# Optimization experiments

Measured on AMD Instinct MI355X. Metric: run time of the kernel, lower is better.

The kernel has to match this reference:

```python
import jax, jax.numpy as jnp
import numpy as np

N_SITES = 100000
DIM = 128
KSIZE = 7  # 7^3 = 343 offsets
GRID = 160


def _build_sparse_structure(seed=0):
    """Sample N_SITES unique voxels in a GRID^3 volume and build the
    depthwise-conv kernel map: neighbor_idx[i, k] = index of site at
    coords[i] + offset[k], or N_SITES (sentinel -> zero row) if absent."""
    rng = np.random.default_rng(seed)
    lin = rng.choice(GRID ** 3, size=N_SITES, replace=False)
    coords = np.stack(np.unravel_index(lin, (GRID, GRID, GRID)), axis=1).astype(np.int64)  # [N,3]
    lookup = np.full(GRID ** 3, N_SITES, dtype=np.int32)
    lookup[lin] = np.arange(N_SITES, dtype=np.int32)
    r = KSIZE // 2
    offs = np.stack(np.meshgrid(*([np.arange(-r, r + 1)] * 3), indexing="ij"), axis=-1).reshape(-1, 3)  # [343,3]
    K = offs.shape[0]
    neighbor_idx = np.full((N_SITES, K), N_SITES, dtype=np.int32)
    for k in range(K):
        nb = coords + offs[k]
        ok = np.all((nb >= 0) & (nb < GRID), axis=1)
        nb_lin = (nb[ok, 0] * GRID + nb[ok, 1]) * GRID + nb[ok, 2]
        neighbor_idx[ok, k] = lookup[nb_lin]
    return neighbor_idx


def setup_inputs() -> dict:
    key = jax.random.key(0)
    ks = jax.random.split(key, 12)
    neighbor_idx = jnp.asarray(_build_sparse_structure(0))
    d, h = DIM, 4 * DIM
    K = KSIZE ** 3
    return {
        "feats": jax.random.normal(ks[0], (N_SITES, d), jnp.float32),
        "neighbor_idx": neighbor_idx,
        "dw_w": jax.random.normal(ks[1], (K, d), jnp.float32) * 0.05,
        "dw_b": jax.random.normal(ks[2], (d,), jnp.float32) * 0.02,
        "ln_g": 1.0 + 0.1 * jax.random.normal(ks[3], (d,), jnp.float32),
        "ln_b": 0.02 * jax.random.normal(ks[4], (d,), jnp.float32),
        "w1": jax.random.normal(ks[5], (d, h), jnp.float32) * (1.0 / np.sqrt(d)),
        "b1": 0.02 * jax.random.normal(ks[6], (h,), jnp.float32),
        "grn_g": 0.1 * jax.random.normal(ks[7], (1, h), jnp.float32),
        "grn_b": 0.02 * jax.random.normal(ks[8], (1, h), jnp.float32),
        "w2": jax.random.normal(ks[9], (h, d), jnp.float32) * (1.0 / np.sqrt(h)),
        "b2": 0.02 * jax.random.normal(ks[10], (d,), jnp.float32),
    }


def reference(feats, neighbor_idx, dw_w, dw_b, ln_g, ln_b, w1, b1, grn_g, grn_b, w2, b2):
    eps = 1e-6
    n, d = feats.shape
    # --- sparse depthwise conv: gather-multiply-accumulate over kernel offsets ---
    f_pad = jnp.concatenate([feats, jnp.zeros((1, d), feats.dtype)], axis=0)  # sentinel row

    def step(acc, xs):
        idx_k, w_k = xs  # idx_k: [N], w_k: [dim]
        return acc + f_pad[idx_k] * w_k, None

    x, _ = jax.lax.scan(step, jnp.zeros_like(feats), (neighbor_idx.T, dw_w))
    x = x + dw_b
    # --- LayerNorm over channels ---
    mu = jnp.mean(x, axis=-1, keepdims=True)
    var = jnp.var(x, axis=-1, keepdims=True)
    x = (x - mu) / jnp.sqrt(var + eps) * ln_g + ln_b
    # --- pwconv1 -> GELU (exact, matching torch default) ---
    x = jax.nn.gelu(x @ w1 + b1, approximate=False)  # [N, 4*dim]
    # --- GRN: L2 norm over all sites (dim=0), per channel ---
    gx = jnp.sqrt(jnp.sum(x * x, axis=0, keepdims=True))  # [1, 4*dim]
    nx = gx / (jnp.mean(gx, axis=-1, keepdims=True) + eps)
    x = grn_g * (x * nx) + grn_b + x
    # --- pwconv2 + residual (drop_path identity in eval) ---
    x = x @ w2 + b2
    return feats + x
```

## Files before the change

kernel.cpp:

```cpp
#include <hip/hip_runtime.h>

typedef unsigned short u16;
typedef unsigned int u32;
typedef __attribute__((ext_vector_type(8))) short bf16x8;
typedef __attribute__((ext_vector_type(4))) float f32x4;

__device__ __forceinline__ u16 f2bf(float f) {
    u32 u = __float_as_uint(f);
    return (u16)((u + 0x7FFFu + ((u >> 16) & 1u)) >> 16);
}

__device__ __forceinline__ float fast_gelu(float x) {
    const float t = x * x;
    const float y2 = x * __builtin_fmaf(0.0713548214f, t, 1.5957691216057308f);
    const float u = __expf(fminf(y2, 80.f));
    return x * u * __builtin_amdgcn_rcpf(u + 1.f);
}

__device__ __forceinline__ void gload_lds16(const u16* g, u16* l) {
    __builtin_amdgcn_global_load_lds(
        (const __attribute__((address_space(1))) void*)g,
        (__attribute__((address_space(3))) void*)l, 16, 0, 0);
}

__global__ __launch_bounds__(256) void cast_feats_k(
    const float* __restrict__ src, u16* __restrict__ dst, int n4)
{
    const int e = blockIdx.x * 256 + threadIdx.x;
    if (e >= n4) return;
    const float4 v = *(const float4*)(src + (size_t)e * 4);
    uint2 o;
    o.x = (u32)f2bf(v.x) | ((u32)f2bf(v.y) << 16);
    o.y = (u32)f2bf(v.z) | ((u32)f2bf(v.w) << 16);
    *(uint2*)(dst + (size_t)e * 4) = o;
}

__global__ __launch_bounds__(256) void dwln_k(
    const u16* __restrict__ featsb, const int* __restrict__ nb,
    const u16* __restrict__ dwwb, const float* __restrict__ dw_b,
    const float* __restrict__ ln_g, const float* __restrict__ ln_b,
    u16* __restrict__ xln, int nsites)
{
    __shared__ int lists[4][352];
    const int w = threadIdx.x >> 6;
    const int lane = threadIdx.x & 63;
    const int s = blockIdx.x * 4 + w;
    if (s >= nsites) return;
    const int* row = nb + (size_t)s * 343;
    int idx[6];
    #pragma unroll
    for (int j = 0; j < 5; ++j) idx[j] = row[lane + j * 64];
    idx[5] = (lane < 23) ? row[320 + lane] : nsites;
    const unsigned long long below = ((1ull << lane) - 1ull);
    int cnt = 0;
    #pragma unroll
    for (int i = 0; i < 6; ++i) {
        const bool v = idx[i] < nsites;
        const unsigned long long bal = __ballot(v);
        const int k = (i < 5) ? (lane + i * 64) : (320 + lane);
        if (v) lists[w][cnt + __popcll(bal & below)] = idx[i] | (k << 17);
        cnt += (int)__popcll(bal);
    }
    const int cntp = (cnt + 7) & ~7;
    if (lane < cntp - cnt) lists[w][cnt + lane] = nsites;
    __builtin_amdgcn_s_waitcnt(0);
    float x0 = 0.f, x1 = 0.f;
    for (int base = 0; base < cntp; base += 8) {
        u32 f[8], wv[8];
        #pragma unroll
        for (int i = 0; i < 8; ++i) {
            const int e = lists[w][base + i];
            f[i]  = *(const u32*)(featsb + (size_t)(e & 0x1FFFF) * 128 + lane * 2);
            wv[i] = *(const u32*)(dwwb + (size_t)(e >> 17) * 128 + lane * 2);
        }
        #pragma unroll
        for (int i = 0; i < 8; ++i) {
            x0 += __uint_as_float(f[i] << 16) * __uint_as_float(wv[i] << 16);
            x1 += __uint_as_float(f[i] & 0xFFFF0000u) * __uint_as_float(wv[i] & 0xFFFF0000u);
        }
    }
    const float2 bv = *(const float2*)(dw_b + lane * 2);
    const float2 gv = *(const float2*)(ln_g + lane * 2);
    const float2 lbv = *(const float2*)(ln_b + lane * 2);
    float a0 = x0 + bv.x, a1 = x1 + bv.y;
    float sm = a0 + a1, ss = a0 * a0 + a1 * a1;
    #pragma unroll
    for (int off = 32; off > 0; off >>= 1) {
        sm += __shfl_xor(sm, off, 64);
        ss += __shfl_xor(ss, off, 64);
    }
    const float mean = sm * (1.f / 128.f);
    const float var = ss * (1.f / 128.f) - mean * mean;
    const float rstd = rsqrtf(fmaxf(var, 0.f) + 1e-6f);
    const float y0 = (a0 - mean) * rstd * gv.x + lbv.x;
    const float y1 = (a1 - mean) * rstd * gv.y + lbv.y;
    *(u32*)(xln + (size_t)s * 128 + lane * 2) =
        (u32)f2bf(y0) | ((u32)f2bf(y1) << 16);
}

__global__ __launch_bounds__(256) void transpose_w1_k(
    const float* __restrict__ w1, u16* __restrict__ w1t)
{
    const int e = blockIdx.x * 256 + threadIdx.x;
    const int n = e >> 7, k = e & 127;
    w1t[e] = f2bf(w1[k * 512 + n]);
}

__global__ __launch_bounds__(256, 4) void gemm1_k(
    const u16* __restrict__ xln, const u16* __restrict__ w1t,
    const float* __restrict__ b1, u16* __restrict__ h,
    float* __restrict__ gx_sq, int nsites, int nmb)
{
    __shared__ u16 xb[2][64 * 128];
    __shared__ float s_red[128];
    const int t = threadIdx.x;
    const int n0 = blockIdx.x * 128;
    const int lane = t & 63;
    const int w = t >> 6;
    const int wn = w * 32;
    const int l15 = lane & 15, quad = lane >> 4;
    if (t < 128) s_red[t] = 0.f;

    #define STAGE1(bsel, mb_)                                                    \
        {                                                                        \
            _Pragma("unroll")                                                    \
            for (int i_ = 0; i_ < 4; ++i_) {                                     \
                const int r_ = w * 16 + i_ * 4 + (lane >> 4);                    \
                const int c_ = (lane & 15) ^ (r_ & 15);                          \
                gload_lds16(xln + (size_t)((mb_) * 64 + r_) * 128 + c_ * 8,      \
                            &xb[bsel][(w * 16 + i_ * 4) * 128]);                 \
            }                                                                    \
        }

    int mb = blockIdx.y;
    STAGE1(0, mb)
    __builtin_amdgcn_sched_barrier(0);
    const u16* a_base = w1t + (size_t)(n0 + wn + l15) * 128 + quad * 8;
    bf16x8 aF[4][2];
    #pragma unroll
    for (int ks = 0; ks < 4; ++ks)
        #pragma unroll
        for (int nt = 0; nt < 2; ++nt)
            aF[ks][nt] = *(const bf16x8*)(a_base + (size_t)nt * 16 * 128 + ks * 32);

    float ssl[2][4] = {{0.f,0.f,0.f,0.f},{0.f,0.f,0.f,0.f}};
    int cur = 0;
    while (mb < nmb) {
        asm volatile("s_waitcnt vmcnt(8)" ::: "memory");
        __builtin_amdgcn_s_barrier();
        __builtin_amdgcn_sched_barrier(0);
        const int mbn = mb + (int)gridDim.y;
        if (mbn < nmb) STAGE1(cur ^ 1, mbn)
        __builtin_amdgcn_sched_barrier(0);
        const int m0 = mb * 64;
        f32x4 acc[2][4];
        #pragma unroll
        for (int i = 0; i < 2; ++i)
            #pragma unroll
            for (int j = 0; j < 4; ++j) acc[i][j] = f32x4{0.f, 0.f, 0.f, 0.f};
        #pragma unroll
        for (int ks = 0; ks < 4; ++ks) {
            bf16x8 b[4];
            #pragma unroll
            for (int mt = 0; mt < 4; ++mt) {
                const int r = mt * 16 + l15;
                b[mt] = *(const bf16x8*)(&xb[cur][r * 128 + (((ks * 4 + quad) ^ l15) << 3)]);
            }
            #pragma unroll
            for (int nt = 0; nt < 2; ++nt)
                #pragma unroll
                for (int mt = 0; mt < 4; ++mt)
                    acc[nt][mt] = __builtin_amdgcn_mfma_f32_16x16x32_bf16(aF[ks][nt], b[mt], acc[nt][mt], 0, 0, 0);
        }
        #pragma unroll
        for (int nt = 0; nt < 2; ++nt) {
            const int chb = n0 + wn + nt * 16 + quad * 4;
            const float4 b1v = *(const float4*)(b1 + chb);
            #pragma unroll
            for (int mt = 0; mt < 4; ++mt) {
                const int site = m0 + mt * 16 + l15;
                if (site < nsites) {
                    float v[4];
                    #pragma unroll
                    for (int rg = 0; rg < 4; ++rg) {
                        v[rg] = fast_gelu(acc[nt][mt][rg] + ((const float*)&b1v)[rg]);
                        ssl[nt][rg] += v[rg] * v[rg];
                    }
                    uint2 o;
                    o.x = (u32)f2bf(v[0]) | ((u32)f2bf(v[1]) << 16);
                    o.y = (u32)f2bf(v[2]) | ((u32)f2bf(v[3]) << 16);
                    *(uint2*)(h + (size_t)site * 512 + chb) = o;
                }
            }
        }
        mb = mbn; cur ^= 1;
    }
    #undef STAGE1
    #pragma unroll
    for (int nt = 0; nt < 2; ++nt)
        #pragma unroll
        for (int rg = 0; rg < 4; ++rg) {
            float v = ssl[nt][rg];
            v += __shfl_xor(v, 1, 64);
            v += __shfl_xor(v, 2, 64);
            v += __shfl_xor(v, 4, 64);
            v += __shfl_xor(v, 8, 64);
            if (l15 == 0) atomicAdd(&s_red[wn + nt * 16 + quad * 4 + rg], v);
        }
    __syncthreads();
    if (t < 128) atomicAdd(&gx_sq[n0 + t], s_red[t]);
}

__global__ __launch_bounds__(256) void beff_k(
    const float* __restrict__ grn_b, const float* __restrict__ w2,
    float* __restrict__ b_eff)
{
    __shared__ float red[256];
    const int t = threadIdx.x;
    const int dc = t & 127, part = t >> 7;
    const int c0 = blockIdx.x * 64 + part * 32;
    float p = 0.f;
    #pragma unroll 8
    for (int i = 0; i < 32; ++i) {
        const int c = c0 + i;
        p += grn_b[c] * w2[(size_t)c * 128 + dc];
    }
    red[t] = p;
    __syncthreads();
    if (t < 128) atomicAdd(&b_eff[t], red[t] + red[t + 128]);
}

__global__ __launch_bounds__(512) void grn_scale_k(
    const float* __restrict__ gx_sq, const float* __restrict__ grn_g,
    float* __restrict__ scale)
{
    __shared__ float red[512];
    const int t = threadIdx.x;
    const float g = sqrtf(gx_sq[t]);
    red[t] = g;
    __syncthreads();
    #pragma unroll
    for (int off = 256; off > 0; off >>= 1) {
        if (t < off) red[t] += red[t + off];
        __syncthreads();
    }
    const float mean = red[0] * (1.f / 512.f);
    scale[t] = grn_g[t] * (g / (mean + 1e-6f)) + 1.f;
}

__global__ __launch_bounds__(256) void w2t_k(
    const float* __restrict__ scale, const float* __restrict__ w2,
    u16* __restrict__ w2t)
{
    const int e = blockIdx.x * 256 + threadIdx.x;
    const int c = e & 511, dc = e >> 9;
    w2t[e] = f2bf(scale[c] * w2[(size_t)c * 128 + dc]);
}

__global__ __launch_bounds__(256, 4) void gemm2_k(
    const u16* __restrict__ h, const u16* __restrict__ w2t,
    const float* __restrict__ b_eff, const float* __restrict__ b2,
    const float* __restrict__ feats,
    float* __restrict__ out, int nsites)
{
    __shared__ u16 hb[2][64 * 128];
    const int t = threadIdx.x;
    const int m0 = blockIdx.x * 64;
    const int lane = t & 63;
    const int w = t >> 6;
    const int wn = w * 32;
    const int l15 = lane & 15, quad = lane >> 4;
    f32x4 acc[2][4];
    #pragma unroll
    for (int i = 0; i < 2; ++i)
        #pragma unroll
        for (int j = 0; j < 4; ++j) acc[i][j] = f32x4{0.f, 0.f, 0.f, 0.f};
    const u16* a_base = w2t + (size_t)(wn + l15) * 512 + quad * 8;

    #define STAGE2(bsel, tc)                                                     \
        {                                                                        \
            _Pragma("unroll")                                                    \
            for (int i_ = 0; i_ < 4; ++i_) {                                     \
                const int r_ = w * 16 + i_ * 4 + (lane >> 4);                    \
                const int c_ = (lane & 15) ^ (r_ & 15);                          \
                gload_lds16(h + (size_t)(m0 + r_) * 512 + (tc) * 128 + c_ * 8,   \
                            &hb[bsel][(w * 16 + i_ * 4) * 128]);                 \
            }                                                                    \
        }

    STAGE2(0, 0)
    bf16x8 aC[2];
    #pragma unroll
    for (int nt = 0; nt < 2; ++nt) aC[nt] = *(const bf16x8*)(a_base + (size_t)nt * 16 * 512);
    asm volatile("s_waitcnt vmcnt(0)" ::: "memory");
    __syncthreads();
    #pragma unroll
    for (int tch = 0; tch < 4; ++tch) {
        const int cur = tch & 1;
        if (tch < 3) STAGE2(cur ^ 1, tch + 1)
        #pragma unroll
        for (int ks = 0; ks < 4; ++ks) {
            const int ksg = tch * 4 + ks;
            bf16x8 aN[2];
            if (ksg < 15) {
                #pragma unroll
                for (int nt = 0; nt < 2; ++nt)
                    aN[nt] = *(const bf16x8*)(a_base + (size_t)nt * 16 * 512 + (ksg + 1) * 32);
            }
            bf16x8 b[4];
            #pragma unroll
            for (int mt = 0; mt < 4; ++mt) {
                const int r = mt * 16 + l15;
                b[mt] = *(const bf16x8*)(&hb[cur][r * 128 + (((ks * 4 + quad) ^ l15) << 3)]);
            }
            #pragma unroll
            for (int nt = 0; nt < 2; ++nt)
                #pragma unroll
                for (int mt = 0; mt < 4; ++mt)
                    acc[nt][mt] = __builtin_amdgcn_mfma_f32_16x16x32_bf16(aC[nt], b[mt], acc[nt][mt], 0, 0, 0);
            if (ksg < 15) {
                #pragma unroll
                for (int nt = 0; nt < 2; ++nt) aC[nt] = aN[nt];
            }
        }
        if (tch < 3) {
            asm volatile("s_waitcnt vmcnt(0)" ::: "memory");
            __syncthreads();
        }
    }
    #undef STAGE2
    #pragma unroll
    for (int nt = 0; nt < 2; ++nt) {
        const int chb = wn + nt * 16 + quad * 4;
        const float4 bev = *(const float4*)(b_eff + chb);
        const float4 b2v = *(const float4*)(b2 + chb);
        #pragma unroll
        for (int mt = 0; mt < 4; ++mt) {
            const int site = m0 + mt * 16 + l15;
            if (site < nsites) {
                const float4 fv = *(const float4*)(feats + (size_t)site * 128 + chb);
                float4 o;
                o.x = acc[nt][mt][0] + bev.x + b2v.x + fv.x;
                o.y = acc[nt][mt][1] + bev.y + b2v.y + fv.y;
                o.z = acc[nt][mt][2] + bev.z + b2v.z + fv.z;
                o.w = acc[nt][mt][3] + bev.w + b2v.w + fv.w;
                *(float4*)(out + (size_t)site * 128 + chb) = o;
            }
        }
    }
}

extern "C" void kernel_launch(void* const* d_in, const int* in_sizes, int n_in,
                              void* d_out, int out_size, void* d_ws, size_t ws_size,
                              hipStream_t stream) {
    const float* feats = (const float*)d_in[0];
    const int* nb      = (const int*)d_in[1];
    const float* dw_w  = (const float*)d_in[2];
    const float* dw_b  = (const float*)d_in[3];
    const float* ln_g  = (const float*)d_in[4];
    const float* ln_b  = (const float*)d_in[5];
    const float* w1    = (const float*)d_in[6];
    const float* b1    = (const float*)d_in[7];
    const float* grn_g = (const float*)d_in[8];
    const float* grn_b = (const float*)d_in[9];
    const float* w2    = (const float*)d_in[10];
    const float* b2    = (const float*)d_in[11];
    float* out = (float*)d_out;
    const int nsites = in_sizes[0] / 128;

    char* ws = (char*)d_ws;
    size_t off = 0;
    u16* xln   = (u16*)(ws + off);  off += (((size_t)(nsites + 128) * 128 * 2) + 255) & ~(size_t)255;
    u16* h     = (u16*)(ws + off);  off += (((size_t)(nsites + 128) * 512 * 2) + 255) & ~(size_t)255;
    u16* featsb= (u16*)(ws + off);  off += (((size_t)(nsites + 1) * 128 * 2) + 255) & ~(size_t)255;
    u16* dwwb  = (u16*)(ws + off);  off += 343 * 128 * 2 + 128;
    u16* w1t   = (u16*)(ws + off);  off += 512 * 128 * 2;
    u16* w2t   = (u16*)(ws + off);  off += 128 * 512 * 2;
    float* gx_sq = (float*)(ws + off); off += 512 * 4;
    float* scale = (float*)(ws + off); off += 512 * 4;
    float* b_eff = (float*)(ws + off); off += 128 * 4;

    hipMemsetAsync(gx_sq, 0, 512 * sizeof(float), stream);
    hipMemsetAsync(b_eff, 0, 128 * sizeof(float), stream);
    hipMemsetAsync(featsb + (size_t)nsites * 128, 0, 128 * sizeof(u16), stream);
    const int nfeat4 = nsites * 32;
    cast_feats_k<<<(nfeat4 + 255) / 256, 256, 0, stream>>>(feats, featsb, nfeat4);
    const int ndww4 = 343 * 32;
    cast_feats_k<<<(ndww4 + 255) / 256, 256, 0, stream>>>(dw_w, dwwb, ndww4);
    transpose_w1_k<<<256, 256, 0, stream>>>(w1, w1t);
    beff_k<<<8, 256, 0, stream>>>(grn_b, w2, b_eff);
    dwln_k<<<(nsites + 3) / 4, 256, 0, stream>>>(featsb, nb, dwwb, dw_b, ln_g, ln_b, xln, nsites);
    const int nmb = (nsites + 63) / 64;
    const int gy = nmb < 256 ? nmb : 256;
    gemm1_k<<<dim3(4, gy), 256, 0, stream>>>(xln, w1t, b1, h, gx_sq, nsites, nmb);
    grn_scale_k<<<1, 512, 0, stream>>>(gx_sq, grn_g, scale);
    w2t_k<<<256, 256, 0, stream>>>(scale, w2, w2t);
    const int m2blocks = (nsites + 63) / 64;
    gemm2_k<<<m2blocks, 256, 0, stream>>>(h, w2t, b_eff, b2, feats, out, nsites);
}
```

Before: 404.1 us.

## Make gemm2 persistent with register-resident weights and cross-tile prefetch

Converts gemm2 into a persistent kernel with a grid capped at 512 blocks that loops over 64-row M tiles. Each wave loads its full slice of the scaled W2 (16x2 bf16x8 fragments) into registers once instead of streaming it per tile. The first h chunk of the next tile is prefetched during the last chunk of the current tile. This is meant to remove repeated weight loads and per-block launch and prologue latency, at the cost of higher register use (occupancy hint lowered to 2) and hand-tuned vmcnt waits that must match the load counts.

```diff
diff --git a/kernel.cpp b/kernel.cpp
--- a/kernel.cpp
+++ b/kernel.cpp
@@ -257,97 +257,114 @@
     w2t[e] = f2bf(scale[c] * w2[(size_t)c * 128 + dc]);
 }
 
-__global__ __launch_bounds__(256, 4) void gemm2_k(
+__global__ __launch_bounds__(256, 2) void gemm2_k(
     const u16* __restrict__ h, const u16* __restrict__ w2t,
     const float* __restrict__ b_eff, const float* __restrict__ b2,
     const float* __restrict__ feats,
-    float* __restrict__ out, int nsites)
+    float* __restrict__ out, int nsites, int nmb)
 {
     __shared__ u16 hb[2][64 * 128];
     const int t = threadIdx.x;
-    const int m0 = blockIdx.x * 64;
     const int lane = t & 63;
     const int w = t >> 6;
     const int wn = w * 32;
     const int l15 = lane & 15, quad = lane >> 4;
-    f32x4 acc[2][4];
-    #pragma unroll
-    for (int i = 0; i < 2; ++i)
-        #pragma unroll
-        for (int j = 0; j < 4; ++j) acc[i][j] = f32x4{0.f, 0.f, 0.f, 0.f};
-    const u16* a_base = w2t + (size_t)(wn + l15) * 512 + quad * 8;
-
-    #define STAGE2(bsel, tc)                                                     \
+
+    #define STAGE2(bsel, mb_, tc)                                                \
         {                                                                        \
             _Pragma("unroll")                                                    \
             for (int i_ = 0; i_ < 4; ++i_) {                                     \
                 const int r_ = w * 16 + i_ * 4 + (lane >> 4);                    \
                 const int c_ = (lane & 15) ^ (r_ & 15);                          \
-                gload_lds16(h + (size_t)(m0 + r_) * 512 + (tc) * 128 + c_ * 8,   \
+                gload_lds16(h + (size_t)((mb_) * 64 + r_) * 512 + (tc) * 128 + c_ * 8, \
                             &hb[bsel][(w * 16 + i_ * 4) * 128]);                 \
             }                                                                    \
         }
-
-    STAGE2(0, 0)
-    bf16x8 aC[2];
-    #pragma unroll
-    for (int nt = 0; nt < 2; ++nt) aC[nt] = *(const bf16x8*)(a_base + (size_t)nt * 16 * 512);
-    asm volatile("s_waitcnt vmcnt(0)" ::: "memory");
-    __syncthreads();
-    #pragma unroll
-    for (int tch = 0; tch < 4; ++tch) {
-        const int cur = tch & 1;
-        if (tch < 3) STAGE2(cur ^ 1, tch + 1)
-        #pragma unroll
-        for (int ks = 0; ks < 4; ++ks) {
-            const int ksg = tch * 4 + ks;
-            bf16x8 aN[2];
-            if (ksg < 15) {
-                #pragma unroll
-                for (int nt = 0; nt < 2; ++nt)
-                    aN[nt] = *(const bf16x8*)(a_base + (size_t)nt * 16 * 512 + (ksg + 1) * 32);
+    #define CHUNK2(bsel, c0ks)                                                   \
+        {                                                                        \
+            _Pragma("unroll")                                                    \
+            for (int ks = 0; ks < 4; ++ks) {                                     \
+                bf16x8 b[4];                                                     \
+                _Pragma("unroll")                                                \
+                for (int mt = 0; mt < 4; ++mt) {                                 \
+                    const int r = mt * 16 + l15;                                 \
+                    b[mt] = *(const bf16x8*)(&hb[bsel][r * 128 + (((ks * 4 + quad) ^ l15) << 3)]); \
+                }                                                                \
+                _Pragma("unroll")                                                \
+                for (int nt = 0; nt < 2; ++nt)                                   \
+                    _Pragma("unroll")                                            \
+                    for (int mt = 0; mt < 4; ++mt)                               \
+                        acc[nt][mt] = __builtin_amdgcn_mfma_f32_16x16x32_bf16(aF[(c0ks) + ks][nt], b[mt], acc[nt][mt], 0, 0, 0); \
+            }                                                                    \
+        }
+
+    int mb = blockIdx.x;
+    STAGE2(0, mb, 0)
+    __builtin_amdgcn_sched_barrier(0);
+    const u16* a_base = w2t + (size_t)(wn + l15) * 512 + quad * 8;
+    bf16x8 aF[16][2];
+    #pragma unroll
+    for (int ks = 0; ks < 16; ++ks)
+        #pragma unroll
+        for (int nt = 0; nt < 2; ++nt)
+            aF[ks][nt] = *(const bf16x8*)(a_base + (size_t)nt * 16 * 512 + ks * 32);
+    __builtin_amdgcn_sched_barrier(0);
+
+    while (mb < nmb) {
+        const int m0 = mb * 64;
+        const int mbn = mb + (int)gridDim.x;
+        f32x4 acc[2][4];
+        #pragma unroll
+        for (int i = 0; i < 2; ++i)
+            #pragma unroll
+            for (int j = 0; j < 4; ++j) acc[i][j] = f32x4{0.f, 0.f, 0.f, 0.f};
+        asm volatile("s_waitcnt vmcnt(16)" ::: "memory");
+        __builtin_amdgcn_s_barrier();
+        __builtin_amdgcn_sched_barrier(0);
+        STAGE2(1, mb, 1)
+        __builtin_amdgcn_sched_barrier(0);
+        CHUNK2(0, 0)
+        asm volatile("s_waitcnt vmcnt(0)" ::: "memory");
+        __builtin_amdgcn_s_barrier();
+        __builtin_amdgcn_sched_barrier(0);
+        STAGE2(0, mb, 2)
+        __builtin_amdgcn_sched_barrier(0);
+        CHUNK2(1, 4)
+        asm volatile("s_waitcnt vmcnt(0)" ::: "memory");
+        __builtin_amdgcn_s_barrier();
+        __builtin_amdgcn_sched_barrier(0);
+        STAGE2(1, mb, 3)
+        __builtin_amdgcn_sched_barrier(0);
+        CHUNK2(0, 8)
+        asm volatile("s_waitcnt vmcnt(0)" ::: "memory");
+        __builtin_amdgcn_s_barrier();
+        __builtin_amdgcn_sched_barrier(0);
+        if (mbn < nmb) STAGE2(0, mbn, 0)
+        __builtin_amdgcn_sched_barrier(0);
+        CHUNK2(1, 12)
+        #pragma unroll
+        for (int nt = 0; nt < 2; ++nt) {
+            const int chb = wn + nt * 16 + quad * 4;
+            const float4 bev = *(const float4*)(b_eff + chb);
+            const float4 b2v = *(const float4*)(b2 + chb);
+            #pragma unroll
+            for (int mt = 0; mt < 4; ++mt) {
+                const int site = m0 + mt * 16 + l15;
+                if (site < nsites) {
+                    const float4 fv = *(const float4*)(feats + (size_t)site * 128 + chb);
+                    float4 o;
+                    o.x = acc[nt][mt][0] + bev.x + b2v.x + fv.x;
+                    o.y = acc[nt][mt][1] + bev.y + b2v.y + fv.y;
+                    o.z = acc[nt][mt][2] + bev.z + b2v.z + fv.z;
+                    o.w = acc[nt][mt][3] + bev.w + b2v.w + fv.w;
+                    *(float4*)(out + (size_t)site * 128 + chb) = o;
+                }
             }
-            bf16x8 b[4];
-            #pragma unroll
-            for (int mt = 0; mt < 4; ++mt) {
-                const int r = mt * 16 + l15;
-                b[mt] = *(const bf16x8*)(&hb[cur][r * 128 + (((ks * 4 + quad) ^ l15) << 3)]);
-            }
-            #pragma unroll
-            for (int nt = 0; nt < 2; ++nt)
-                #pragma unroll
-                for (int mt = 0; mt < 4; ++mt)
-                    acc[nt][mt] = __builtin_amdgcn_mfma_f32_16x16x32_bf16(aC[nt], b[mt], acc[nt][mt], 0, 0, 0);
-            if (ksg < 15) {
-                #pragma unroll
-                for (int nt = 0; nt < 2; ++nt) aC[nt] = aN[nt];
-            }
-        }
-        if (tch < 3) {
-            asm volatile("s_waitcnt vmcnt(0)" ::: "memory");
-            __syncthreads();
-        }
+        }
+        mb = mbn;
     }
     #undef STAGE2
-    #pragma unroll
-    for (int nt = 0; nt < 2; ++nt) {
-        const int chb = wn + nt * 16 + quad * 4;
-        const float4 bev = *(const float4*)(b_eff + chb);
-        const float4 b2v = *(const float4*)(b2 + chb);
-        #pragma unroll
-        for (int mt = 0; mt < 4; ++mt) {
-            const int site = m0 + mt * 16 + l15;
-            if (site < nsites) {
-                const float4 fv = *(const float4*)(feats + (size_t)site * 128 + chb);
-                float4 o;
-                o.x = acc[nt][mt][0] + bev.x + b2v.x + fv.x;
-                o.y = acc[nt][mt][1] + bev.y + b2v.y + fv.y;
-                o.z = acc[nt][mt][2] + bev.z + b2v.z + fv.z;
-                o.w = acc[nt][mt][3] + bev.w + b2v.w + fv.w;
-                *(float4*)(out + (size_t)site * 128 + chb) = o;
-            }
-        }
-    }
+    #undef CHUNK2
 }
 
 extern "C" void kernel_launch(void* const* d_in, const int* in_sizes, int n_in,
@@ -395,6 +412,6 @@
     gemm1_k<<<dim3(4, gy), 256, 0, stream>>>(xln, w1t, b1, h, gx_sq, nsites, nmb);
     grn_scale_k<<<1, 512, 0, stream>>>(gx_sq, grn_g, scale);
     w2t_k<<<256, 256, 0, stream>>>(scale, w2, w2t);
-    const int m2blocks = (nsites + 63) / 64;
-    gemm2_k<<<m2blocks, 256, 0, stream>>>(h, w2t, b_eff, b2, feats, out, nsites);
-}
+    const int g2 = nmb < 512 ? nmb : 512;
+    gemm2_k<<<g2, 256, 0, stream>>>(h, w2t, b_eff, b2, feats, out, nsites, nmb);
+}
```

New measurement: 404.2 us. No clear change (+0.0%).
